# Kernel tuning notes

Hardware: AMD Instinct MI355X
Metric: run time of the kernel (lower is better)

## Reference

```python
import jax, jax.numpy as jnp
import numpy as np

D_MODEL = 1024
HEADS = 16
D_HEAD = D_MODEL // HEADS


def setup_inputs() -> dict:
    key = jax.random.key(0)
    ks = jax.random.split(key, 5)
    B, S = 4, 2048
    x = jax.random.normal(ks[0], (B, S, D_MODEL), dtype=jnp.float32)
    # nn.Linear weights are [out, in]; store as [in, out] for x @ W convention
    s_qkv = 1.0 / np.sqrt(D_MODEL)
    w_qkv = jax.random.uniform(ks[1], (D_MODEL, 3 * D_MODEL), jnp.float32, -s_qkv, s_qkv)
    b_qkv = jax.random.uniform(ks[2], (3 * D_MODEL,), jnp.float32, -s_qkv, s_qkv)
    w_proj = jax.random.uniform(ks[3], (D_MODEL, D_MODEL), jnp.float32, -s_qkv, s_qkv)
    b_proj = jax.random.uniform(ks[4], (D_MODEL,), jnp.float32, -s_qkv, s_qkv)
    return {"x": x, "w_qkv": w_qkv, "b_qkv": b_qkv, "w_proj": w_proj, "b_proj": b_proj}


def reference(x, w_qkv, b_qkv, w_proj, b_proj):
    B, S, D = x.shape
    scale = D_HEAD ** (-0.5)
    qkv = x @ w_qkv + b_qkv                        # [B,S,3D]
    qkv = qkv.reshape(B, S, 3, HEADS, D_HEAD)
    qkv = jnp.transpose(qkv, (2, 0, 3, 1, 4))      # [3,B,H,S,dh]
    q, k, v = qkv[0], qkv[1], qkv[2]
    attn = jnp.einsum("bhsd,bhtd->bhst", q, k) * scale
    attn = jax.nn.softmax(attn, axis=-1)
    ctx = jnp.einsum("bhst,bhtd->bhsd", attn, v)   # [B,H,S,dh]
    ctx = jnp.transpose(ctx, (0, 2, 1, 3)).reshape(B, S, D)
    return ctx @ w_proj + b_proj
```

## Files before the change

### kernel.cpp

```cpp
#include <hip/hip_runtime.h>

typedef unsigned short u16;
typedef unsigned int u32;
typedef __attribute__((ext_vector_type(8))) short short8;
typedef __attribute__((ext_vector_type(4))) float f32x4;
typedef __attribute__((ext_vector_type(2))) unsigned int u32x2;

extern "C" __device__ float __ocml_native_exp2_f32(float);

__device__ __forceinline__ u16 f32_to_bf16(float f) {
  u32 u = __builtin_bit_cast(u32, f);
  u += 0x7fffu + ((u >> 16) & 1u);
  return (u16)(u >> 16);
}

__device__ __forceinline__ u32 cvt_pk_bf16(float a, float b) {
  u32 r;
  asm("v_cvt_pk_bf16_f32 %0, %1, %2" : "=v"(r) : "v"(a), "v"(b));
  return r;
}

__device__ __forceinline__ void gload16(const void* g, void* l) {
  __builtin_amdgcn_global_load_lds((const __attribute__((address_space(1))) u32*)g,
                                   (__attribute__((address_space(3))) u32*)l, 16, 0, 0);
}

__global__ __launch_bounds__(256) void cvt_bf16_kernel(const float* __restrict__ in,
                                                       u16* __restrict__ out, int n8) {
  int i = blockIdx.x * 256 + threadIdx.x;
  if (i >= n8) return;
  const float4* p = (const float4*)in + (size_t)i * 2;
  float4 a = p[0], b = p[1];
  int4 v;
  v.x = (int)f32_to_bf16(a.x) | ((int)f32_to_bf16(a.y) << 16);
  v.y = (int)f32_to_bf16(a.z) | ((int)f32_to_bf16(a.w) << 16);
  v.z = (int)f32_to_bf16(b.x) | ((int)f32_to_bf16(b.y) << 16);
  v.w = (int)f32_to_bf16(b.z) | ((int)f32_to_bf16(b.w) << 16);
  *(int4*)(out + (size_t)i * 8) = v;
}

__global__ __launch_bounds__(256) void transpose_bf16_kernel(const float* __restrict__ in,
                                                             u16* __restrict__ out, int R, int C) {
  __shared__ u16 tile[32][33];
  int tx = threadIdx.x & 31, ty = threadIdx.x >> 5;
  int c0 = blockIdx.x * 32, r0 = blockIdx.y * 32;
#pragma unroll
  for (int j = 0; j < 32; j += 8)
    tile[ty + j][tx] = f32_to_bf16(in[(size_t)(r0 + ty + j) * C + c0 + tx]);
  __syncthreads();
#pragma unroll
  for (int j = 0; j < 32; j += 8)
    out[(size_t)(c0 + ty + j) * R + r0 + tx] = tile[tx][ty + j];
}

template <int MODE>
__global__ __launch_bounds__(256) void gemm_kernel(
    const u16* __restrict__ A, const u16* __restrict__ Bt, const float* __restrict__ bias,
    float* __restrict__ outf, u16* __restrict__ qo, u16* __restrict__ ko, u16* __restrict__ vo,
    int M, int N, int K) {
  __shared__ u16 Sm[2][2][4096];
  const int tid = threadIdx.x;
  const int id = blockIdx.y * gridDim.x + blockIdx.x;
  const int nwg = gridDim.x * gridDim.y;
  const int swz = (id & 7) * (nwg >> 3) + (id >> 3);
  const int bn = (swz % gridDim.x) * 128;
  const int bm = (swz / gridDim.x) * 128;
  const int lane = tid & 63, wid = tid >> 6;
  const int lo = lane & 15, hi = lane >> 4;
  const int wm = (wid >> 1) * 64, wn = (wid & 1) * 64;
  const int srow = lane >> 2, schk = lane & 3;
  const u16* as0 = A + (size_t)(bm + wid * 32 + srow) * K + schk * 8;
  const u16* bs0 = Bt + (size_t)(bn + wid * 32 + srow) * K + schk * 8;
  const size_t row16 = (size_t)16 * K;

  f32x4 acc[4][4] = {};
  gload16(as0, &Sm[0][0][wid * 1024]);
  gload16(as0 + row16, &Sm[0][0][wid * 1024 + 512]);
  gload16(bs0, &Sm[0][1][wid * 1024]);
  gload16(bs0 + row16, &Sm[0][1][wid * 1024 + 512]);
  int cur = 0;
  for (int k0 = 0; k0 < K; k0 += 32) {
    __syncthreads();
    if (k0 + 32 < K) {
      int nx = cur ^ 1;
      gload16(as0 + k0 + 32, &Sm[nx][0][wid * 1024]);
      gload16(as0 + k0 + 32 + row16, &Sm[nx][0][wid * 1024 + 512]);
      gload16(bs0 + k0 + 32, &Sm[nx][1][wid * 1024]);
      gload16(bs0 + k0 + 32 + row16, &Sm[nx][1][wid * 1024 + 512]);
    }
    const u16* Al = Sm[cur][0];
    const u16* Bl = Sm[cur][1];
    short8 af[4], bfr[4];
#pragma unroll
    for (int mi = 0; mi < 4; ++mi) af[mi] = *(const short8*)&Al[(wm + mi * 16 + lo) * 32 + hi * 8];
#pragma unroll
    for (int ni = 0; ni < 4; ++ni) bfr[ni] = *(const short8*)&Bl[(wn + ni * 16 + lo) * 32 + hi * 8];
#pragma unroll
    for (int mi = 0; mi < 4; ++mi)
#pragma unroll
      for (int ni = 0; ni < 4; ++ni)
        acc[mi][ni] = __builtin_amdgcn_mfma_f32_16x16x32_bf16(af[mi], bfr[ni], acc[mi][ni], 0, 0, 0);
    cur ^= 1;
  }

  if (MODE == 0 && bn >= 2048) {
    u16* T = &Sm[0][0][0];
    const int b = bm >> 11;
    const int sbase = bm & 2047;
#pragma unroll
    for (int hh = 0; hh < 2; ++hh) {
      __syncthreads();
      if (wn == hh * 64) {
#pragma unroll
        for (int ni = 0; ni < 4; ++ni) {
          int c = ni * 16 + lo;
          float bv = bias[bn + hh * 64 + c];
#pragma unroll
          for (int mi = 0; mi < 4; ++mi) {
            u32* dst = (u32*)&T[c * 136 + wm + mi * 16 + hi * 4];
            dst[0] = cvt_pk_bf16(acc[mi][ni][0] + bv, acc[mi][ni][1] + bv);
            dst[1] = cvt_pk_bf16(acc[mi][ni][2] + bv, acc[mi][ni][3] + bv);
          }
        }
      }
      __syncthreads();
      int h = ((bn - 2048) >> 6) + hh;
#pragma unroll
      for (int p = 0; p < 4; ++p) {
        int unit = p * 256 + tid;
        int c = unit >> 4, chunk = unit & 15;
        short8 v = *(const short8*)&T[c * 136 + chunk * 8];
        *(short8*)&vo[((size_t)((b * 16 + h) * 64 + c)) * 2048 + sbase + chunk * 8] = v;
      }
    }
  } else {
#pragma unroll
    for (int mi = 0; mi < 4; ++mi)
#pragma unroll
      for (int ni = 0; ni < 4; ++ni) {
        int col = bn + wn + ni * 16 + lo;
        float bv = bias[col];
#pragma unroll
        for (int r = 0; r < 4; ++r) {
          int row = bm + wm + mi * 16 + hi * 4 + r;
          float val = acc[mi][ni][r] + bv;
          if (MODE == 1) {
            outf[(size_t)row * N + col] = val;
          } else {
            int part = col >> 10, rem = col & 1023;
            int h = rem >> 6, d = rem & 63;
            int b = row >> 11, s = row & 2047;
            if (part == 0)
              qo[((size_t)(b * 16 + h) * 2048 + s) * 64 + d] = f32_to_bf16(val);
            else
              ko[((size_t)(b * 16 + h) * 2048 + s) * 64 + d] = f32_to_bf16(val);
          }
        }
      }
  }
}

__global__ __launch_bounds__(256, 3) void attn_kernel(const u16* __restrict__ Qg,
                                                      const u16* __restrict__ Kg,
                                                      const u16* __restrict__ Vtg,
                                                      u16* __restrict__ ctx) {
  __shared__ u16 KV[2][2][4096];
  __shared__ u16 Pb[4][2304];
  const int tid = threadIdx.x;
  const int lane = tid & 63, wid = tid >> 6;
  const int lo = lane & 15, hi = lane >> 4;
  const int id = blockIdx.y * gridDim.x + blockIdx.x;
  const int swz = (id & 7) * 128 + (id >> 3);
  const int qb = swz & 15, bh = swz >> 4;
  const u16* Qh = Qg + (size_t)bh * (2048 * 64);
  const u16* Kh = Kg + (size_t)bh * (2048 * 64);
  const u16* Vh = Vtg + (size_t)bh * (64 * 2048);

  short8 qf[2][2];
#pragma unroll
  for (int ni = 0; ni < 2; ++ni)
#pragma unroll
    for (int kk = 0; kk < 2; ++kk)
      qf[ni][kk] = *(const short8*)&Qh[(size_t)(qb * 128 + wid * 32 + ni * 16 + lo) * 64 +
                                       kk * 32 + hi * 8];

  const int srow = lane >> 3;
  const int schk = (lane & 7) ^ srow;
  const u16* ksrc = Kh + (size_t)(wid * 16 + srow) * 64 + schk * 8;
  const u16* vsrc = Vh + (size_t)(wid * 16 + srow) * 2048 + schk * 8;

  const short8 ONES = {0x3F80, 0x3F80, 0x3F80, 0x3F80, 0x3F80, 0x3F80, 0x3F80, 0x3F80};
  f32x4 o[2][4] = {};
  f32x4 lst[2] = {};
  float msx0 = -3.0e38f, msx1 = -3.0e38f;
  const float C = 0.18033688f;

#define STAGE(buf, kt)                                                     \
  do {                                                                     \
    gload16(ksrc + (size_t)(kt) * 4096, &KV[buf][0][wid * 1024]);          \
    gload16(ksrc + (size_t)(kt) * 4096 + 512, &KV[buf][0][wid * 1024 + 512]); \
    gload16(vsrc + (size_t)(kt) * 64, &KV[buf][1][wid * 1024]);            \
    gload16(vsrc + (size_t)(kt) * 64 + 8 * 2048, &KV[buf][1][wid * 1024 + 512]); \
  } while (0)

  STAGE(0, 0);
  int cur = 0;
  for (int kt = 0; kt < 32; ++kt) {
    __syncthreads();
    if (kt < 31) STAGE(cur ^ 1, kt + 1);
    const u16* Ks = KV[cur][0];
    const u16* Vs = KV[cur][1];

    f32x4 sa[4][2] = {};
#pragma unroll
    for (int kk = 0; kk < 2; ++kk) {
      short8 kf[4];
#pragma unroll
      for (int mi = 0; mi < 4; ++mi)
        kf[mi] = *(const short8*)&Ks[(mi * 16 + lo) * 64 + (((kk * 4 + hi) ^ (lo & 7)) * 8)];
      __builtin_amdgcn_s_setprio(1);
#pragma unroll
      for (int mi = 0; mi < 4; ++mi)
#pragma unroll
        for (int ni = 0; ni < 2; ++ni)
          sa[mi][ni] = __builtin_amdgcn_mfma_f32_16x16x32_bf16(kf[mi], qf[ni][kk], sa[mi][ni], 0, 0, 0);
      __builtin_amdgcn_s_setprio(0);
    }

    float mx0 = fmaxf(fmaxf(sa[0][0][0], sa[0][0][1]), fmaxf(sa[0][0][2], sa[0][0][3]));
    float mx1 = fmaxf(fmaxf(sa[0][1][0], sa[0][1][1]), fmaxf(sa[0][1][2], sa[0][1][3]));
#pragma unroll
    for (int mi = 1; mi < 4; ++mi) {
      mx0 = fmaxf(mx0, fmaxf(fmaxf(sa[mi][0][0], sa[mi][0][1]), fmaxf(sa[mi][0][2], sa[mi][0][3])));
      mx1 = fmaxf(mx1, fmaxf(fmaxf(sa[mi][1][0], sa[mi][1][1]), fmaxf(sa[mi][1][2], sa[mi][1][3])));
    }
    mx0 = fmaxf(mx0, __shfl_xor(mx0, 16, 64));
    mx0 = fmaxf(mx0, __shfl_xor(mx0, 32, 64));
    mx1 = fmaxf(mx1, __shfl_xor(mx1, 16, 64));
    mx1 = fmaxf(mx1, __shfl_xor(mx1, 32, 64));

    int grow = (mx0 > msx0 + 64.f) | (mx1 > msx1 + 64.f);
    if (__any(grow)) {
      float mn0 = fmaxf(msx0, mx0), mn1 = fmaxf(msx1, mx1);
      float c0 = __ocml_native_exp2_f32((msx0 - mn0) * C);
      float c1 = __ocml_native_exp2_f32((msx1 - mn1) * C);
      msx0 = mn0;
      msx1 = mn1;
#pragma unroll
      for (int qi = 0; qi < 2; ++qi)
#pragma unroll
        for (int r = 0; r < 4; ++r) {
          float cf = __shfl(qi == 0 ? c0 : c1, hi * 4 + r, 64);
          lst[qi][r] *= cf;
#pragma unroll
          for (int di = 0; di < 4; ++di) o[qi][di][r] *= cf;
        }
    }
    float mc0 = msx0 * C, mc1 = msx1 * C;
#pragma unroll
    for (int mi = 0; mi < 4; ++mi)
#pragma unroll
      for (int ni = 0; ni < 2; ++ni)
#pragma unroll
        for (int r = 0; r < 4; ++r)
          sa[mi][ni][r] = __ocml_native_exp2_f32(__builtin_fmaf(sa[mi][ni][r], C, ni ? -mc1 : -mc0));

#pragma unroll
    for (int mi = 0; mi < 4; ++mi)
#pragma unroll
      for (int ni = 0; ni < 2; ++ni) {
        u32x2 w;
        w.x = cvt_pk_bf16(sa[mi][ni][0], sa[mi][ni][1]);
        w.y = cvt_pk_bf16(sa[mi][ni][2], sa[mi][ni][3]);
        *(u32x2*)&Pb[wid][(ni * 16 + lo) * 72 + mi * 16 + hi * 4] = w;
      }
    asm volatile("s_waitcnt lgkmcnt(0)" ::: "memory");
    __builtin_amdgcn_sched_barrier(0);

#pragma unroll
    for (int kk2 = 0; kk2 < 2; ++kk2) {
      short8 pf[2], vf[4];
#pragma unroll
      for (int qi = 0; qi < 2; ++qi)
        pf[qi] = *(const short8*)&Pb[wid][(qi * 16 + lo) * 72 + kk2 * 32 + hi * 8];
#pragma unroll
      for (int di = 0; di < 4; ++di)
        vf[di] = *(const short8*)&Vs[(di * 16 + lo) * 64 + (((kk2 * 4 + hi) ^ (lo & 7)) * 8)];
      __builtin_amdgcn_s_setprio(1);
#pragma unroll
      for (int qi = 0; qi < 2; ++qi)
        lst[qi] = __builtin_amdgcn_mfma_f32_16x16x32_bf16(pf[qi], ONES, lst[qi], 0, 0, 0);
#pragma unroll
      for (int qi = 0; qi < 2; ++qi)
#pragma unroll
        for (int di = 0; di < 4; ++di)
          o[qi][di] = __builtin_amdgcn_mfma_f32_16x16x32_bf16(pf[qi], vf[di], o[qi][di], 0, 0, 0);
      __builtin_amdgcn_s_setprio(0);
    }
    cur ^= 1;
  }
#undef STAGE

  int b = bh >> 4, h = bh & 15;
#pragma unroll
  for (int qi = 0; qi < 2; ++qi)
#pragma unroll
    for (int r = 0; r < 4; ++r) {
      float inv = __builtin_amdgcn_rcpf(lst[qi][r]);
      int sr = qb * 128 + wid * 32 + qi * 16 + hi * 4 + r;
      u16* crow = ctx + (size_t)(b * 2048 + sr) * 1024 + h * 64;
#pragma unroll
      for (int di = 0; di < 4; ++di) crow[di * 16 + lo] = f32_to_bf16(o[qi][di][r] * inv);
    }
}

extern "C" void kernel_launch(void* const* d_in, const int* in_sizes, int n_in,
                              void* d_out, int out_size, void* d_ws, size_t ws_size,
                              hipStream_t stream) {
  const float* x      = (const float*)d_in[0];
  const float* w_qkv  = (const float*)d_in[1];
  const float* b_qkv  = (const float*)d_in[2];
  const float* w_proj = (const float*)d_in[3];
  const float* b_proj = (const float*)d_in[4];
  float* out = (float*)d_out;
  char* ws = (char*)d_ws;

  u16* xb     = (u16*)(ws);
  u16* wqkvT  = (u16*)(ws + 16777216);
  u16* wprojT = (u16*)(ws + 23068672);
  u16* Vt     = (u16*)(ws + 25165824);
  u16* Q = (u16*)d_out;
  u16* K = Q + 8388608;

  cvt_bf16_kernel<<<4096, 256, 0, stream>>>(x, xb, 1048576);
  transpose_bf16_kernel<<<dim3(96, 32), 256, 0, stream>>>(w_qkv, wqkvT, 1024, 3072);
  transpose_bf16_kernel<<<dim3(32, 32), 256, 0, stream>>>(w_proj, wprojT, 1024, 1024);
  gemm_kernel<0><<<dim3(24, 64), 256, 0, stream>>>(xb, wqkvT, b_qkv, nullptr, Q, K, Vt,
                                                   8192, 3072, 1024);
  attn_kernel<<<dim3(16, 64), 256, 0, stream>>>(Q, K, Vt, xb);
  gemm_kernel<1><<<dim3(8, 64), 256, 0, stream>>>(xb, wprojT, b_proj, out,
                                                  nullptr, nullptr, nullptr, 8192, 1024, 1024);
}
```

Before: 291.7 us.

## Replace QKV GEMM with 256x256-tile 8-wave kernel and swizzled LDS epilogue

Adds a dedicated QKV projection kernel with 256x256 output tiles, 512 threads, and a multi-phase double-buffered global-to-LDS pipeline with XOR-swizzled LDS layout and explicit vmcnt waits. The Q/K/V epilogue is staged through LDS so stores to the head-major Q/K and transposed V buffers are 16-byte coalesced. The aim is to raise data reuse per loaded tile, avoid LDS bank conflicts, and remove the scattered 2-byte Q/K stores of the old epilogue. It costs more registers and LDS per block and relies on hand-tuned wait counts that are fixed to this problem shape.

```diff
diff --git a/kernel.cpp b/kernel.cpp
--- a/kernel.cpp
+++ b/kernel.cpp
@@ -53,11 +53,145 @@
     out[(size_t)(c0 + ty + j) * R + r0 + tx] = tile[tx][ty + j];
 }
 
+__global__ __launch_bounds__(512, 2) void gemm256_kernel(
+    const u16* __restrict__ A, const u16* __restrict__ Bt, const float* __restrict__ bias,
+    u16* __restrict__ qo, u16* __restrict__ ko, u16* __restrict__ vo) {
+  __shared__ u16 lds[2][2][2][8192];
+  const int tid = threadIdx.x;
+  const int lane = tid & 63, w = tid >> 6;
+  const int lo = lane & 15, hi = lane >> 4;
+  const int wr = w >> 2, wn4 = w & 3;
+  const int id = blockIdx.y * gridDim.x + blockIdx.x;
+  const int swz = (id & 7) * 48 + (id >> 3);
+  const int bn = (swz % 12) * 256, bm = (swz / 12) * 256;
+  const int srow4 = lane >> 2;
+  const int scol = (lane & 3) ^ ((lane >> 3) & 3);
+  const u16* aRow = A + (size_t)(bm + w * 16 + srow4) * 1024 + scol * 8;
+  const u16* bRow = Bt + (size_t)(bn + w * 16 + srow4) * 1024 + scol * 8;
+  const int achk = (hi ^ ((lo >> 1) & 3)) * 8;
+  const int bro = wn4 * 64;
+
+  f32x4 acc[8][4] = {};
+
+#define STG(sdb, sab, shk, tile)                                      \
+  if ((tile) < 16) {                                                  \
+    const u16* g = ((sab) ? bRow : aRow) + (tile) * 64 + (shk) * 32;  \
+    u16* d = &lds[sdb][sab][shk][w * 512];                            \
+    gload16(g, d);                                                    \
+    gload16(g + 128 * 1024, d + 4096);                                \
+  }
+
+#define W8 asm volatile("s_waitcnt vmcnt(8)" ::: "memory")
+#define W4 asm volatile("s_waitcnt vmcnt(4)" ::: "memory")
+#define W0 asm volatile("s_waitcnt vmcnt(0)" ::: "memory")
+#define WN ((void)0)
+
+  STG(0, 0, 0, 0); STG(0, 1, 0, 0); STG(0, 0, 1, 0); STG(0, 1, 1, 0);
+  STG(1, 0, 0, 1); STG(1, 1, 0, 1);
+  W8;
+  __builtin_amdgcn_s_barrier();
+
+#define PHASE(db, MH, KK, sdb, sab, shk, tile, WAITOP)                                           \
+  {                                                                                              \
+    short8 af[4], bf[4];                                                                         \
+    _Pragma("unroll") for (int m4 = 0; m4 < 4; ++m4)                                             \
+      af[m4] = *(const short8*)&lds[db][0][KK][(wr * 128 + MH * 64 + m4 * 16 + lo) * 32 + achk]; \
+    _Pragma("unroll") for (int ni = 0; ni < 4; ++ni)                                             \
+      bf[ni] = *(const short8*)&lds[db][1][KK][(bro + ni * 16 + lo) * 32 + achk];                \
+    STG(sdb, sab, shk, tile);                                                                    \
+    WAITOP;                                                                                      \
+    __builtin_amdgcn_s_barrier();                                                                \
+    asm volatile("s_waitcnt lgkmcnt(0)" ::: "memory");                                           \
+    __builtin_amdgcn_sched_barrier(0);                                                           \
+    __builtin_amdgcn_s_setprio(1);                                                               \
+    _Pragma("unroll") for (int m4 = 0; m4 < 4; ++m4)                                             \
+      _Pragma("unroll") for (int ni = 0; ni < 4; ++ni)                                           \
+        acc[MH * 4 + m4][ni] = __builtin_amdgcn_mfma_f32_16x16x32_bf16(                          \
+            af[m4], bf[ni], acc[MH * 4 + m4][ni], 0, 0, 0);                                      \
+    __builtin_amdgcn_s_setprio(0);                                                               \
+    __builtin_amdgcn_s_barrier();                                                                \
+  }
+
+  for (int i = 0; i < 7; ++i) {
+    const int t1 = 2 * i + 1, t2 = 2 * i + 2, t3 = 2 * i + 3;
+    PHASE(0, 0, 0, 1, 0, 1, t1, WN);
+    PHASE(0, 1, 0, 1, 1, 1, t1, W8);
+    PHASE(0, 0, 1, 0, 0, 0, t2, WN);
+    PHASE(0, 1, 1, 0, 1, 0, t2, W8);
+    PHASE(1, 0, 0, 0, 0, 1, t2, WN);
+    PHASE(1, 1, 0, 0, 1, 1, t2, W8);
+    PHASE(1, 0, 1, 1, 0, 0, t3, WN);
+    PHASE(1, 1, 1, 1, 1, 0, t3, W8);
+  }
+  PHASE(0, 0, 0, 1, 0, 1, 15, WN);
+  PHASE(0, 1, 0, 1, 1, 1, 15, W8);
+  PHASE(0, 0, 1, 0, 0, 0, 16, WN);
+  PHASE(0, 1, 1, 0, 1, 0, 16, W4);
+  PHASE(1, 0, 0, 0, 0, 1, 16, WN);
+  PHASE(1, 1, 0, 0, 1, 1, 16, W0);
+  PHASE(1, 0, 1, 1, 0, 0, 17, WN);
+  PHASE(1, 1, 1, 1, 1, 0, 17, WN);
+#undef PHASE
+#undef STG
+
+  u16* T = &lds[0][0][0][0] + w * 8192;
+  const int colbase = bn + wn4 * 64;
+  const int part = colbase >> 10;
+  const int h = (colbase & 1023) >> 6;
+  const int grow0 = bm + wr * 128;
+  const int b = grow0 >> 11;
+  const int s0 = grow0 & 2047;
+  float bv[4];
+#pragma unroll
+  for (int ni = 0; ni < 4; ++ni) bv[ni] = bias[colbase + ni * 16 + lo];
+
+  if (part < 2) {
+#pragma unroll
+    for (int mi = 0; mi < 8; ++mi)
+#pragma unroll
+      for (int ni = 0; ni < 4; ++ni) {
+        const int col = ni * 16 + lo;
+#pragma unroll
+        for (int r = 0; r < 4; ++r) {
+          const int row = mi * 16 + hi * 4 + r;
+          T[row * 64 + (((col >> 3) ^ (row & 7)) * 8) + (col & 7)] =
+              f32_to_bf16(acc[mi][ni][r] + bv[ni]);
+        }
+      }
+    u16* dst = part ? ko : qo;
+#pragma unroll
+    for (int rr = 0; rr < 16; ++rr) {
+      const int row = rr * 8 + (lane >> 3);
+      const int c = lane & 7;
+      short8 v = *(const short8*)&T[row * 64 + (((c ^ (row & 7)) * 8))];
+      *(short8*)&dst[((size_t)(b * 16 + h) * 2048 + s0 + row) * 64 + c * 8] = v;
+    }
+  } else {
+#pragma unroll
+    for (int mi = 0; mi < 8; ++mi)
+#pragma unroll
+      for (int ni = 0; ni < 4; ++ni) {
+        const int d = ni * 16 + lo;
+        u32x2 wv;
+        wv.x = cvt_pk_bf16(acc[mi][ni][0] + bv[ni], acc[mi][ni][1] + bv[ni]);
+        wv.y = cvt_pk_bf16(acc[mi][ni][2] + bv[ni], acc[mi][ni][3] + bv[ni]);
+        const int chunk = 2 * mi + (hi >> 1);
+        *(u32x2*)&T[d * 128 + ((chunk ^ (d & 15)) * 8) + (hi & 1) * 4] = wv;
+      }
+#pragma unroll
+    for (int rr = 0; rr < 16; ++rr) {
+      const int u = rr * 64 + lane;
+      const int d = u >> 4, c = u & 15;
+      short8 v = *(const short8*)&T[d * 128 + ((c ^ (d & 15)) * 8)];
+      *(short8*)&vo[((size_t)(b * 16 + h) * 64 + d) * 2048 + s0 + c * 8] = v;
+    }
+  }
+}
+
 template <int MODE>
 __global__ __launch_bounds__(256) void gemm_kernel(
     const u16* __restrict__ A, const u16* __restrict__ Bt, const float* __restrict__ bias,
-    float* __restrict__ outf, u16* __restrict__ qo, u16* __restrict__ ko, u16* __restrict__ vo,
-    int M, int N, int K) {
+    float* __restrict__ outf, int M, int N, int K) {
   __shared__ u16 Sm[2][2][4096];
   const int tid = threadIdx.x;
   const int id = blockIdx.y * gridDim.x + blockIdx.x;
@@ -103,61 +237,18 @@
     cur ^= 1;
   }
 
-  if (MODE == 0 && bn >= 2048) {
-    u16* T = &Sm[0][0][0];
-    const int b = bm >> 11;
-    const int sbase = bm & 2047;
-#pragma unroll
-    for (int hh = 0; hh < 2; ++hh) {
-      __syncthreads();
-      if (wn == hh * 64) {
-#pragma unroll
-        for (int ni = 0; ni < 4; ++ni) {
-          int c = ni * 16 + lo;
-          float bv = bias[bn + hh * 64 + c];
-#pragma unroll
-          for (int mi = 0; mi < 4; ++mi) {
-            u32* dst = (u32*)&T[c * 136 + wm + mi * 16 + hi * 4];
-            dst[0] = cvt_pk_bf16(acc[mi][ni][0] + bv, acc[mi][ni][1] + bv);
-            dst[1] = cvt_pk_bf16(acc[mi][ni][2] + bv, acc[mi][ni][3] + bv);
-          }
-        }
+#pragma unroll
+  for (int mi = 0; mi < 4; ++mi)
+#pragma unroll
+    for (int ni = 0; ni < 4; ++ni) {
+      int col = bn + wn + ni * 16 + lo;
+      float bvv = bias[col];
+#pragma unroll
+      for (int r = 0; r < 4; ++r) {
+        int row = bm + wm + mi * 16 + hi * 4 + r;
+        outf[(size_t)row * N + col] = acc[mi][ni][r] + bvv;
       }
-      __syncthreads();
-      int h = ((bn - 2048) >> 6) + hh;
-#pragma unroll
-      for (int p = 0; p < 4; ++p) {
-        int unit = p * 256 + tid;
-        int c = unit >> 4, chunk = unit & 15;
-        short8 v = *(const short8*)&T[c * 136 + chunk * 8];
-        *(short8*)&vo[((size_t)((b * 16 + h) * 64 + c)) * 2048 + sbase + chunk * 8] = v;
-      }
-    }
-  } else {
-#pragma unroll
-    for (int mi = 0; mi < 4; ++mi)
-#pragma unroll
-      for (int ni = 0; ni < 4; ++ni) {
-        int col = bn + wn + ni * 16 + lo;
-        float bv = bias[col];
-#pragma unroll
-        for (int r = 0; r < 4; ++r) {
-          int row = bm + wm + mi * 16 + hi * 4 + r;
-          float val = acc[mi][ni][r] + bv;
-          if (MODE == 1) {
-            outf[(size_t)row * N + col] = val;
-          } else {
-            int part = col >> 10, rem = col & 1023;
-            int h = rem >> 6, d = rem & 63;
-            int b = row >> 11, s = row & 2047;
-            if (part == 0)
-              qo[((size_t)(b * 16 + h) * 2048 + s) * 64 + d] = f32_to_bf16(val);
-            else
-              ko[((size_t)(b * 16 + h) * 2048 + s) * 64 + d] = f32_to_bf16(val);
-          }
-        }
-      }
-  }
+    }
 }
 
 __global__ __launch_bounds__(256, 3) void attn_kernel(const u16* __restrict__ Qg,
@@ -269,10 +360,10 @@
     for (int mi = 0; mi < 4; ++mi)
 #pragma unroll
       for (int ni = 0; ni < 2; ++ni) {
-        u32x2 w;
-        w.x = cvt_pk_bf16(sa[mi][ni][0], sa[mi][ni][1]);
-        w.y = cvt_pk_bf16(sa[mi][ni][2], sa[mi][ni][3]);
-        *(u32x2*)&Pb[wid][(ni * 16 + lo) * 72 + mi * 16 + hi * 4] = w;
+        u32x2 wv;
+        wv.x = cvt_pk_bf16(sa[mi][ni][0], sa[mi][ni][1]);
+        wv.y = cvt_pk_bf16(sa[mi][ni][2], sa[mi][ni][3]);
+        *(u32x2*)&Pb[wid][(ni * 16 + lo) * 72 + mi * 16 + hi * 4] = wv;
       }
     asm volatile("s_waitcnt lgkmcnt(0)" ::: "memory");
     __builtin_amdgcn_sched_barrier(0);
@@ -335,9 +426,7 @@
   cvt_bf16_kernel<<<4096, 256, 0, stream>>>(x, xb, 1048576);
   transpose_bf16_kernel<<<dim3(96, 32), 256, 0, stream>>>(w_qkv, wqkvT, 1024, 3072);
   transpose_bf16_kernel<<<dim3(32, 32), 256, 0, stream>>>(w_proj, wprojT, 1024, 1024);
-  gemm_kernel<0><<<dim3(24, 64), 256, 0, stream>>>(xb, wqkvT, b_qkv, nullptr, Q, K, Vt,
-                                                   8192, 3072, 1024);
+  gemm256_kernel<<<dim3(12, 32), 512, 0, stream>>>(xb, wqkvT, b_qkv, Q, K, Vt);
   attn_kernel<<<dim3(16, 64), 256, 0, stream>>>(Q, K, Vt, xb);
-  gemm_kernel<1><<<dim3(8, 64), 256, 0, stream>>>(xb, wprojT, b_proj, out,
-                                                  nullptr, nullptr, nullptr, 8192, 1024, 1024);
-}
+  gemm_kernel<1><<<dim3(8, 64), 256, 0, stream>>>(xb, wprojT, b_proj, out, 8192, 1024, 1024);
+}
```

Result: no change. 291.8 us (+0.0%).
